# Kernel optimization log

Hardware: AMD Instinct MI355X
Metric: run time of the kernel (lower is better)

The kernel has to match this reference:

```python
import jax, jax.numpy as jnp
import numpy as np

N_NODES = 50000
N_EDGES = 600000
N_GRAPHS = 128
EMB = 128
LAYERS = 5
BN_EPS = 1e-5


def setup_inputs() -> dict:
    key = jax.random.key(0)
    ks = jax.random.split(key, 16)
    inp = {}
    inp['batch'] = jnp.sort(jax.random.randint(ks[0], (N_NODES,), 0, N_GRAPHS)).astype(jnp.int64 if jax.config.jax_enable_x64 else jnp.int32)
    inp['x'] = jax.random.normal(ks[1], (N_NODES, 48), dtype=jnp.float32)
    inp['edge_index'] = jax.random.randint(ks[2], (2, N_EDGES), 0, N_NODES)
    inp['edge_attr'] = jax.random.normal(ks[3], (N_EDGES, 11), dtype=jnp.float32)
    inp['edge_weight'] = jnp.ones((N_EDGES,), dtype=jnp.float32)
    # parameters (xavier-ish scaling)
    inp['W_atom'] = jax.random.normal(ks[4], (48, EMB), dtype=jnp.float32) * (1.0 / np.sqrt(48))
    inp['b_atom'] = jnp.zeros((EMB,), dtype=jnp.float32)
    inp['W_bond'] = jax.random.normal(ks[5], (11, EMB), dtype=jnp.float32) * (1.0 / np.sqrt(11))
    inp['b_bond'] = jnp.zeros((EMB,), dtype=jnp.float32)
    inp['Wl'] = jax.random.normal(ks[6], (LAYERS, EMB, EMB), dtype=jnp.float32) * (1.0 / np.sqrt(EMB))
    inp['bl'] = jnp.zeros((LAYERS, EMB), dtype=jnp.float32)
    inp['Wr'] = jax.random.normal(ks[7], (LAYERS, EMB, EMB), dtype=jnp.float32) * (1.0 / np.sqrt(EMB))
    inp['gamma'] = jnp.ones((LAYERS, EMB), dtype=jnp.float32)
    inp['beta'] = jnp.zeros((LAYERS, EMB), dtype=jnp.float32)
    return inp


def reference(batch, x, edge_index, edge_attr, edge_weight,
              W_atom, b_atom, W_bond, b_bond, Wl, bl, Wr, gamma, beta):
    src = edge_index[0]
    dst = edge_index[1]
    # encoders
    h = x @ W_atom + b_atom                      # [N, EMB]
    ea = edge_attr @ W_bond + b_bond             # [E, EMB]
    # mean-aggregation denominator (in-degree, count-based)
    deg = jax.ops.segment_sum(jnp.ones_like(edge_weight), dst, num_segments=N_NODES)
    denom = jnp.maximum(deg, 1.0)[:, None]       # [N, 1]
    xs = []
    for i in range(LAYERS):
        # SAGEConv: mean over (x_j + edge_attr) * w_e, then lin_l(agg) + lin_r(x)
        msg = (h[src] + ea) * edge_weight[:, None]          # [E, EMB]
        agg = jax.ops.segment_sum(msg, dst, num_segments=N_NODES) / denom
        h = agg @ Wl[i] + bl[i] + h @ Wr[i]
        # BatchNorm1d (training: batch statistics, biased variance)
        mu = jnp.mean(h, axis=0)
        var = jnp.var(h, axis=0)
        h = gamma[i] * (h - mu) * jax.lax.rsqrt(var + BN_EPS) + beta[i]
        if i < LAYERS - 1:
            h = jax.nn.relu(h)
        # dropout with drop_ratio=0.0 is identity
        xs.append(h)
    # layerwise global_add_pool + concat
    xpool = jnp.concatenate(
        [jax.ops.segment_sum(xi, batch, num_segments=N_GRAPHS) for xi in xs], axis=1)
    return (xpool, h)
```

## Files before the change

### kernel.cpp

```cpp
#include <hip/hip_runtime.h>
#include <hip/hip_bf16.h>

#define NNODES 50000
#define NEDGES 600000
#define NGRAPHS 128
#define EMB 128
#define NLAYERS 5
#define BN_EPS 1e-5f
#define SCAN_BLOCKS ((NNODES + 255) / 256)
#define NSB ((NNODES + 255) / 256)
#define EAB ((NNODES + 31) / 32)
#define BPB ((NLAYERS * 32768 + 255) / 256)
#define POOL_CH ((NNODES + 255) / 256)

typedef short s16x8 __attribute__((ext_vector_type(8)));
typedef float f32x16 __attribute__((ext_vector_type(16)));

__device__ __forceinline__ short f2bf(float f) {
    unsigned u = __builtin_bit_cast(unsigned, f);
    unsigned r = (u + 0x7fffu + ((u >> 16) & 1u)) >> 16;
    return (short)r;
}
__device__ __forceinline__ float bf2f(short s) {
    return __builtin_bit_cast(float, ((unsigned)(unsigned short)s) << 16);
}

__global__ __launch_bounds__(256) void init_kernel(float* __restrict__ pool,
                                                   int* __restrict__ deg,
                                                   float* __restrict__ stat) {
    int i = blockIdx.x * 256 + threadIdx.x;
    if (i < NGRAPHS * 640) pool[i] = 0.f;
    if (i < NNODES) deg[i] = 0;
    if (i < NLAYERS * 256) stat[i] = 0.f;
}

__global__ __launch_bounds__(256) void deg_kernel(const int* __restrict__ ei,
                                                  int* __restrict__ deg) {
    int e = blockIdx.x * 256 + threadIdx.x;
    if (e >= NEDGES) return;
    atomicAdd(&deg[ei[NEDGES + e]], 1);
}

__global__ __launch_bounds__(256) void scan1(const int* __restrict__ deg,
                                             int* __restrict__ local_excl,
                                             int* __restrict__ part) {
    __shared__ int sh[256];
    int t = threadIdx.x;
    int i = blockIdx.x * 256 + t;
    int v = (i < NNODES) ? deg[i] : 0;
    sh[t] = v;
    __syncthreads();
    for (int off = 1; off < 256; off <<= 1) {
        int u = (t >= off) ? sh[t - off] : 0;
        __syncthreads();
        sh[t] += u;
        __syncthreads();
    }
    if (i < NNODES) local_excl[i] = sh[t] - v;
    if (t == 255) part[blockIdx.x] = sh[255];
}

__global__ __launch_bounds__(256) void scan23(const int* __restrict__ part,
                                              const int* __restrict__ local_excl,
                                              int* __restrict__ rowptr,
                                              int* __restrict__ cursor) {
    __shared__ int sh[256];
    int t = threadIdx.x;
    int v = (t < SCAN_BLOCKS) ? part[t] : 0;
    sh[t] = v;
    __syncthreads();
    for (int off = 1; off < 256; off <<= 1) {
        int u = (t >= off) ? sh[t - off] : 0;
        __syncthreads();
        sh[t] += u;
        __syncthreads();
    }
    int bo = (blockIdx.x == 0) ? 0 : sh[blockIdx.x - 1];
    int i = blockIdx.x * 256 + t;
    if (i < NNODES) {
        int r = local_excl[i] + bo;
        rowptr[i] = r;
        cursor[i] = r;
    }
    if (blockIdx.x == 0 && t == 0) rowptr[NNODES] = sh[SCAN_BLOCKS - 1];
}

__global__ __launch_bounds__(256) void edge_fill(const int* __restrict__ ei,
                                                 const float* __restrict__ ew,
                                                 const float* __restrict__ eattr,
                                                 int* __restrict__ cursor,
                                                 int* __restrict__ epk) {
    int e = blockIdx.x * 256 + threadIdx.x;
    if (e >= NEDGES) return;
    int src = ei[e];
    int dst = ei[NEDGES + e];
    int pos = atomicAdd(&cursor[dst], 1);
    int pk[8];
    pk[0] = src;
    pk[1] = __float_as_int(ew[e]);
    unsigned short a[12];
#pragma unroll
    for (int j = 0; j < 11; j++) a[j] = (unsigned short)f2bf(eattr[e * 11 + j]);
    a[11] = 0;
#pragma unroll
    for (int j = 0; j < 6; j++)
        pk[2 + j] = (int)a[2 * j] | ((int)a[2 * j + 1] << 16);
    int* dstp = epk + (size_t)pos * 8;
    *(int4*)dstp = *(int4*)pk;
    *(int4*)(dstp + 4) = *(int4*)(pk + 4);
}

__global__ __launch_bounds__(256) void prep2(const int* __restrict__ rowptr,
                                             const int* __restrict__ epk,
                                             int2* __restrict__ epg,
                                             const float* __restrict__ Wb,
                                             const float* __restrict__ bbond,
                                             short* __restrict__ Ehi,
                                             const float* __restrict__ X,
                                             const float* __restrict__ Wa,
                                             const float* __restrict__ ba,
                                             short* __restrict__ Hhi,
                                             const float* __restrict__ Wl,
                                             const float* __restrict__ Wr,
                                             short* __restrict__ Bf) {
    __shared__ float shpool[1792];
    int blk = blockIdx.x;
    int t = threadIdx.x;

    if (blk < NSB) {
        float* Wb_s = shpool;
        float* bb_s = shpool + 1408;
        for (int i = t; i < 1408; i += 256) Wb_s[i] = Wb[i];
        if (t < 128) bb_s[t] = bbond[t];
        __syncthreads();
        int node = blk * 256 + t;
        if (node >= NNODES) return;
        int b = rowptr[node], e = rowptr[node + 1];
        float s[11];
#pragma unroll
        for (int j = 0; j < 11; j++) s[j] = 0.f;
        float ws = 0.f;
        for (int p = b; p < e; p++) {
            const int* pk = epk + (size_t)p * 8;
            int4 lo = *(const int4*)pk;
            int4 hi = *(const int4*)(pk + 4);
            float w = __int_as_float(lo.y);
            ws += w;
            epg[p] = make_int2(lo.x, lo.y);
            int packed[6] = {lo.z, lo.w, hi.x, hi.y, hi.z, hi.w};
#pragma unroll
            for (int j = 0; j < 11; j++) {
                short v = (short)((packed[j >> 1] >> ((j & 1) * 16)) & 0xffff);
                s[j] += bf2f(v) * w;
            }
        }
        short* erow = Ehi + (size_t)node * 128;
#pragma unroll
        for (int c8 = 0; c8 < 16; c8++) {
            s16x8 o;
#pragma unroll
            for (int jj = 0; jj < 8; jj++) {
                int c = c8 * 8 + jj;
                float a = bb_s[c] * ws;
#pragma unroll
                for (int j = 0; j < 11; j++) a += s[j] * Wb_s[j * 128 + c];
                o[jj] = f2bf(a);
            }
            *(s16x8*)(erow + c8 * 8) = o;
        }
    } else if (blk < NSB + EAB) {
        float* as = shpool;
        int row0 = (blk - NSB) * 32;
        for (int i = t; i < 32 * 48; i += 256) {
            int r = i / 48, k = i - r * 48;
            int gr = row0 + r;
            as[k * 36 + r] = (gr < NNODES) ? X[gr * 48 + k] : 0.f;
        }
        __syncthreads();
        int c = t & 127, rh = t >> 7;
        float acc[16];
#pragma unroll
        for (int i = 0; i < 16; i++) acc[i] = 0.f;
        for (int k = 0; k < 48; k++) {
            float w = Wa[k * 128 + c];
            const float* rowv = &as[k * 36 + rh * 16];
            float4 v0 = *(const float4*)(rowv + 0);
            float4 v1 = *(const float4*)(rowv + 4);
            float4 v2 = *(const float4*)(rowv + 8);
            float4 v3 = *(const float4*)(rowv + 12);
            acc[0] += v0.x * w;  acc[1] += v0.y * w;
            acc[2] += v0.z * w;  acc[3] += v0.w * w;
            acc[4] += v1.x * w;  acc[5] += v1.y * w;
            acc[6] += v1.z * w;  acc[7] += v1.w * w;
            acc[8] += v2.x * w;  acc[9] += v2.y * w;
            acc[10] += v2.z * w; acc[11] += v2.w * w;
            acc[12] += v3.x * w; acc[13] += v3.y * w;
            acc[14] += v3.z * w; acc[15] += v3.w * w;
        }
        float bb = ba[c];
        for (int i = 0; i < 16; i++) {
            int gr = row0 + rh * 16 + i;
            if (gr < NNODES) Hhi[(size_t)gr * 128 + c] = f2bf(acc[i] + bb);
        }
    } else {
        int idx = (blk - NSB - EAB) * 256 + t;
        if (idx >= NLAYERS * 32768) return;
        int layer = idx >> 15;
        int r = idx & 32767;
        int k = r >> 7, col = r & 127;
        float w = (k < 128) ? Wl[layer * 16384 + k * 128 + col]
                            : Wr[layer * 16384 + (k - 128) * 128 + col];
        short hi = f2bf(w);
        short lo = f2bf(w - bf2f(hi));
        int ks = k >> 4, half = (k >> 3) & 1, j = k & 7;
        int nt = col >> 5, n32 = col & 31;
        int fo = ((nt * 2 + half) * 32 + n32) * 8 + j;
        short* base = Bf + (size_t)layer * 65536 + ks * 4096;
        base[fo] = hi;
        base[2048 + fo] = lo;
    }
}

__global__ __launch_bounds__(256) void agg_kernel(const short* __restrict__ Hsrc,
                                                  const short* __restrict__ Ehi,
                                                  const int* __restrict__ rowptr,
                                                  const int2* __restrict__ epg,
                                                  const float* __restrict__ stat,
                                                  const float* __restrict__ gamma,
                                                  const float* __restrict__ beta,
                                                  short* __restrict__ Ahi) {
    __shared__ float cscs[128], cshs[128];
    int t = threadIdx.x;
    if (t < 128) {
        float sc = 1.f, sh = 0.f;
        if (stat) {
            const float invM = 1.f / (float)NNODES;
            float mu = stat[t] * invM;
            float var = stat[128 + t] * invM - mu * mu;
            sc = gamma[t] * rsqrtf(var + BN_EPS);
            sh = beta[t] - mu * sc;
        }
        cscs[t] = sc;
        cshs[t] = sh;
    }
    __syncthreads();
    int lane = t & 15, grp = t >> 4;
    int c8 = lane * 8;
    int node = blockIdx.x * 16 + grp;
    if (node >= NNODES) return;
    float rlo = stat ? 0.f : -3.4e38f;
    float sc[8], sh[8];
#pragma unroll
    for (int j = 0; j < 8; j++) { sc[j] = cscs[c8 + j]; sh[j] = cshs[c8 + j]; }
    int b = rowptr[node], e = rowptr[node + 1];
    float s[8];
#pragma unroll
    for (int j = 0; j < 8; j++) s[j] = 0.f;
    int p = b;
    for (; p + 3 < e; p += 4) {
        int2 e0 = epg[p], e1 = epg[p + 1], e2 = epg[p + 2], e3 = epg[p + 3];
        float w0 = __int_as_float(e0.y), w1 = __int_as_float(e1.y);
        float w2 = __int_as_float(e2.y), w3 = __int_as_float(e3.y);
        s16x8 h0 = *(const s16x8*)&Hsrc[(size_t)e0.x * 128 + c8];
        s16x8 h1 = *(const s16x8*)&Hsrc[(size_t)e1.x * 128 + c8];
        s16x8 h2 = *(const s16x8*)&Hsrc[(size_t)e2.x * 128 + c8];
        s16x8 h3 = *(const s16x8*)&Hsrc[(size_t)e3.x * 128 + c8];
#pragma unroll
        for (int j = 0; j < 8; j++) {
            float v0 = fmaxf(bf2f(h0[j]) * sc[j] + sh[j], rlo);
            float v1 = fmaxf(bf2f(h1[j]) * sc[j] + sh[j], rlo);
            float v2 = fmaxf(bf2f(h2[j]) * sc[j] + sh[j], rlo);
            float v3 = fmaxf(bf2f(h3[j]) * sc[j] + sh[j], rlo);
            s[j] += v0 * w0 + v1 * w1 + v2 * w2 + v3 * w3;
        }
    }
    for (; p < e; p++) {
        int2 pk0 = epg[p];
        float w0 = __int_as_float(pk0.y);
        s16x8 h0 = *(const s16x8*)&Hsrc[(size_t)pk0.x * 128 + c8];
#pragma unroll
        for (int j = 0; j < 8; j++)
            s[j] += fmaxf(bf2f(h0[j]) * sc[j] + sh[j], rlo) * w0;
    }
    float inv = 1.f / fmaxf((float)(e - b), 1.f);
    s16x8 ea = *(const s16x8*)&Ehi[(size_t)node * 128 + c8];
    s16x8 o;
#pragma unroll
    for (int j = 0; j < 8; j++) o[j] = f2bf((s[j] + bf2f(ea[j])) * inv);
    *(s16x8*)&Ahi[(size_t)node * 128 + c8] = o;
}

__global__ __launch_bounds__(256) void layer_gemm(const short* __restrict__ Ahi,
                                                  const short* __restrict__ Hsrc,
                                                  const float* __restrict__ statp,
                                                  const float* __restrict__ gamma,
                                                  const float* __restrict__ beta,
                                                  const short* __restrict__ Bf,
                                                  const float* __restrict__ bias,
                                                  short* __restrict__ Cbf,
                                                  float* __restrict__ stat) {
    __shared__ float s_s[128], s_q[128];
    __shared__ float csc[128], csh[128];
    int t = threadIdx.x;
    int wave = t >> 6, lane = t & 63;
    int n32 = lane & 31, half = lane >> 5;
    int rowgrp = wave >> 1, colgrp = wave & 1;
    int row0 = blockIdx.x * 64 + rowgrp * 32;

    if (t < 128) {
        s_s[t] = 0.f;
        s_q[t] = 0.f;
        float sc = 1.f, sh = 0.f;
        if (statp) {
            const float invM = 1.f / (float)NNODES;
            float mu = statp[t] * invM;
            float var = statp[128 + t] * invM - mu * mu;
            sc = gamma[t] * rsqrtf(var + BN_EPS);
            sh = beta[t] - mu * sc;
        }
        csc[t] = sc;
        csh[t] = sh;
    }
    __syncthreads();
    float rlo = statp ? 0.f : -3.4e38f;

    int myrow = row0 + n32;
    bool rowok = myrow < NNODES;
    size_t rbase = (size_t)myrow * 128;
    int acol = half * 8;

    f32x16 acc[2];
#pragma unroll
    for (int i = 0; i < 2; i++) acc[i] = (f32x16)(0.f);

    const short* bb0 = Bf + colgrp * 1024 + half * 256 + n32 * 8;

    s16x8 ahA = {0, 0, 0, 0, 0, 0, 0, 0}, ahB = {0, 0, 0, 0, 0, 0, 0, 0};
    s16x8 bhA[2], blA[2], bhB[2], blB[2];
    if (rowok) {
        ahA = *(const s16x8*)(Ahi + rbase + acol);
        ahB = *(const s16x8*)(Ahi + rbase + 16 + acol);
    }
#pragma unroll
    for (int nt = 0; nt < 2; nt++) {
        bhA[nt] = *(const s16x8*)(bb0 + nt * 512);
        blA[nt] = *(const s16x8*)(bb0 + 2048 + nt * 512);
        bhB[nt] = *(const s16x8*)(bb0 + 4096 + nt * 512);
        blB[nt] = *(const s16x8*)(bb0 + 4096 + 2048 + nt * 512);
    }

#pragma unroll
    for (int ks = 0; ks < 16; ks++) {
        s16x8 ahC = {0, 0, 0, 0, 0, 0, 0, 0};
        s16x8 bhC[2], blC[2];
        if (ks < 14) {
            int kn = ks + 2;
            if (rowok) {
                if (kn < 8) {
                    ahC = *(const s16x8*)(Ahi + rbase + kn * 16 + acol);
                } else {
                    s16x8 hv = *(const s16x8*)(Hsrc + rbase + (kn & 7) * 16 + acol);
                    int kc = (kn & 7) * 16 + acol;
#pragma unroll
                    for (int j = 0; j < 8; j++)
                        ahC[j] = f2bf(fmaxf(bf2f(hv[j]) * csc[kc + j] +
                                            csh[kc + j], rlo));
                }
            }
            const short* bbn = bb0 + kn * 4096;
#pragma unroll
            for (int nt = 0; nt < 2; nt++) {
                bhC[nt] = *(const s16x8*)(bbn + nt * 512);
                blC[nt] = *(const s16x8*)(bbn + 2048 + nt * 512);
            }
        }
#pragma unroll
        for (int nt = 0; nt < 2; nt++) {
            acc[nt] = __builtin_amdgcn_mfma_f32_32x32x16_bf16(ahA, bhA[nt], acc[nt], 0, 0, 0);
            acc[nt] = __builtin_amdgcn_mfma_f32_32x32x16_bf16(ahA, blA[nt], acc[nt], 0, 0, 0);
        }
        ahA = ahB;
        ahB = ahC;
#pragma unroll
        for (int nt = 0; nt < 2; nt++) {
            bhA[nt] = bhB[nt];
            blA[nt] = blB[nt];
            bhB[nt] = bhC[nt];
            blB[nt] = blC[nt];
        }
    }

#pragma unroll
    for (int nt = 0; nt < 2; nt++) {
        int col = colgrp * 64 + nt * 32 + n32;
        float bb = bias[col];
        float ss = 0.f, qq = 0.f;
#pragma unroll
        for (int reg = 0; reg < 16; reg++) {
            int r = row0 + (reg & 3) + 8 * (reg >> 2) + 4 * half;
            if (r < NNODES) {
                float v = acc[nt][reg] + bb;
                Cbf[(size_t)r * 128 + col] = f2bf(v);
                ss += v;
                qq += v * v;
            }
        }
        ss += __shfl_xor(ss, 32);
        qq += __shfl_xor(qq, 32);
        if (half == 0) {
            atomicAdd(&s_s[col], ss);
            atomicAdd(&s_q[col], qq);
        }
    }
    __syncthreads();
    if (t < 128) {
        atomicAdd(&stat[t], s_s[t]);
        atomicAdd(&stat[128 + t], s_q[t]);
    }
}

__global__ __launch_bounds__(256) void pool5(const short* __restrict__ Cbf,
                                             const float* __restrict__ stat,
                                             const float* __restrict__ gamma,
                                             const float* __restrict__ beta,
                                             const int* __restrict__ batch,
                                             float* __restrict__ pool,
                                             float* __restrict__ Hf32) {
    __shared__ float csc[128], csh[128];
    int t = threadIdx.x;
    int u = blockIdx.x;
    int ch = u / NLAYERS, l = u - ch * NLAYERS;
    if (t < 128) {
        const float invM = 1.f / (float)NNODES;
        float mu = stat[l * 256 + t] * invM;
        float var = stat[l * 256 + 128 + t] * invM - mu * mu;
        float sc = gamma[l * 128 + t] * rsqrtf(var + BN_EPS);
        csc[t] = sc;
        csh[t] = beta[l * 128 + t] - mu * sc;
    }
    __syncthreads();
    int lane = t & 31, grp = t >> 5;
    int c4 = lane * 4;
    float4 sc = *(const float4*)&csc[c4];
    float4 sh = *(const float4*)&csh[c4];
    const short* Cl = Cbf + (size_t)l * NNODES * 128;
    int row0 = ch * 256;
    float4 accp = make_float4(0.f, 0.f, 0.f, 0.f);
    int curg = -1;
    float* pbase = pool + l * 128 + c4;
    int relu = (l < NLAYERS - 1);
    for (int rr = grp; rr < 256; rr += 8) {
        int r = row0 + rr;
        if (r >= NNODES) break;
        ushort4 cv = *(const ushort4*)&Cl[(size_t)r * 128 + c4];
        float4 v;
        v.x = bf2f((short)cv.x) * sc.x + sh.x;
        v.y = bf2f((short)cv.y) * sc.y + sh.y;
        v.z = bf2f((short)cv.z) * sc.z + sh.z;
        v.w = bf2f((short)cv.w) * sc.w + sh.w;
        if (relu) {
            v.x = fmaxf(v.x, 0.f);
            v.y = fmaxf(v.y, 0.f);
            v.z = fmaxf(v.z, 0.f);
            v.w = fmaxf(v.w, 0.f);
        } else {
            *(float4*)&Hf32[(size_t)r * 128 + c4] = v;
        }
        int g = batch[r];
        if (g != curg) {
            if (curg >= 0) {
                float* p = pbase + curg * 640;
                atomicAdd(p + 0, accp.x);
                atomicAdd(p + 1, accp.y);
                atomicAdd(p + 2, accp.z);
                atomicAdd(p + 3, accp.w);
            }
            curg = g;
            accp = make_float4(0.f, 0.f, 0.f, 0.f);
        }
        accp.x += v.x;
        accp.y += v.y;
        accp.z += v.z;
        accp.w += v.w;
    }
    if (curg >= 0) {
        float* p = pbase + curg * 640;
        atomicAdd(p + 0, accp.x);
        atomicAdd(p + 1, accp.y);
        atomicAdd(p + 2, accp.z);
        atomicAdd(p + 3, accp.w);
    }
}

extern "C" void kernel_launch(void* const* d_in, const int* in_sizes, int n_in,
                              void* d_out, int out_size, void* d_ws, size_t ws_size,
                              hipStream_t stream) {
    const int* batch = (const int*)d_in[0];
    const float* x = (const float*)d_in[1];
    const int* edge_index = (const int*)d_in[2];
    const float* edge_attr = (const float*)d_in[3];
    const float* edge_weight = (const float*)d_in[4];
    const float* W_atom = (const float*)d_in[5];
    const float* b_atom = (const float*)d_in[6];
    const float* W_bond = (const float*)d_in[7];
    const float* b_bond = (const float*)d_in[8];
    const float* Wl = (const float*)d_in[9];
    const float* bl = (const float*)d_in[10];
    const float* Wr = (const float*)d_in[11];
    const float* gamma = (const float*)d_in[12];
    const float* beta = (const float*)d_in[13];
    float* out = (float*)d_out;

    char* ws = (char*)d_ws;
    size_t off = 0;
    auto alloc = [&](size_t bytes) -> void* {
        void* p = ws + off;
        off += (bytes + 255) & ~(size_t)255;
        return p;
    };
    short* Hhi = (short*)alloc((size_t)NNODES * 128 * 2);
    short* Ahi = (short*)alloc((size_t)NNODES * 128 * 2);
    short* Ehi = (short*)alloc((size_t)NNODES * 128 * 2);
    short* Cbf = (short*)alloc((size_t)NLAYERS * NNODES * 128 * 2);
    int* epk = (int*)alloc((size_t)NEDGES * 32);
    int2* epg = (int2*)alloc((size_t)NEDGES * 8);
    int* rowptr = (int*)alloc((size_t)(NNODES + 1) * 4);
    int* cursor = (int*)alloc((size_t)NNODES * 4);
    int* deg = (int*)alloc((size_t)NNODES * 4);
    float* stat = (float*)alloc(NLAYERS * 256 * 4);
    int* local_excl = (int*)alloc((size_t)NNODES * 4);
    int* part = (int*)alloc(SCAN_BLOCKS * 4);
    short* Bf = (short*)alloc((size_t)NLAYERS * 65536 * 2);

    init_kernel<<<(NGRAPHS * 640 + 255) / 256, 256, 0, stream>>>(out, deg, stat);
    deg_kernel<<<(NEDGES + 255) / 256, 256, 0, stream>>>(edge_index, deg);
    scan1<<<SCAN_BLOCKS, 256, 0, stream>>>(deg, local_excl, part);
    scan23<<<SCAN_BLOCKS, 256, 0, stream>>>(part, local_excl, rowptr, cursor);
    edge_fill<<<(NEDGES + 255) / 256, 256, 0, stream>>>(edge_index, edge_weight,
                                                        edge_attr, cursor, epk);
    prep2<<<NSB + EAB + BPB, 256, 0, stream>>>(rowptr, epk, epg, W_bond, b_bond, Ehi,
                                               x, W_atom, b_atom, Hhi, Wl, Wr, Bf);

    const short* src = Hhi;
    for (int i = 0; i < NLAYERS; i++) {
        const float* st = (i == 0) ? nullptr : stat + (i - 1) * 256;
        const float* gm = (i == 0) ? nullptr : gamma + (i - 1) * 128;
        const float* bt = (i == 0) ? nullptr : beta + (i - 1) * 128;
        short* Ci = Cbf + (size_t)i * NNODES * 128;
        agg_kernel<<<(NNODES + 15) / 16, 256, 0, stream>>>(src, Ehi, rowptr, epg,
                                                           st, gm, bt, Ahi);
        layer_gemm<<<(NNODES + 63) / 64, 256, 0, stream>>>(
            Ahi, src, st, gm, bt, Bf + (size_t)i * 65536, bl + i * 128, Ci,
            stat + i * 256);
        src = Ci;
    }

    pool5<<<POOL_CH * NLAYERS, 256, 0, stream>>>(
        Cbf, stat, gamma, beta, batch, out, out + (size_t)NGRAPHS * 640);
}
```

Before: 588.2 us.

## Widen GEMM tile to full 128 columns, spread BN stat atomics, cache batch ids

The layer GEMM now has each wave compute all 128 output columns for 32 rows, so a block covers 128 rows and the A row fetch and BN-transform work is no longer duplicated across two column groups. The change doubles the accumulator and B-fragment register footprint per wave, which may reduce occupancy. BatchNorm statistic atomics are spread over 8 slots per layer to cut contention, and every reader sums the slots. The pooling kernel also stages batch indices in shared memory before its row loop.

```diff
diff --git a/kernel.cpp b/kernel.cpp
--- a/kernel.cpp
+++ b/kernel.cpp
@@ -7,6 +7,7 @@
 #define EMB 128
 #define NLAYERS 5
 #define BN_EPS 1e-5f
+#define STATW 8
 #define SCAN_BLOCKS ((NNODES + 255) / 256)
 #define NSB ((NNODES + 255) / 256)
 #define EAB ((NNODES + 31) / 32)
@@ -23,6 +24,16 @@
 }
 __device__ __forceinline__ float bf2f(short s) {
     return __builtin_bit_cast(float, ((unsigned)(unsigned short)s) << 16);
+}
+
+__device__ __forceinline__ float2 stat_sum(const float* __restrict__ st, int t) {
+    float s = 0.f, q = 0.f;
+#pragma unroll
+    for (int k = 0; k < STATW; k++) {
+        s += st[k * 256 + t];
+        q += st[k * 256 + 128 + t];
+    }
+    return make_float2(s, q);
 }
 
 __global__ __launch_bounds__(256) void init_kernel(float* __restrict__ pool,
@@ -31,7 +42,7 @@
     int i = blockIdx.x * 256 + threadIdx.x;
     if (i < NGRAPHS * 640) pool[i] = 0.f;
     if (i < NNODES) deg[i] = 0;
-    if (i < NLAYERS * 256) stat[i] = 0.f;
+    if (i < NLAYERS * STATW * 256) stat[i] = 0.f;
 }
 
 __global__ __launch_bounds__(256) void deg_kernel(const int* __restrict__ ei,
@@ -235,8 +246,9 @@
         float sc = 1.f, sh = 0.f;
         if (stat) {
             const float invM = 1.f / (float)NNODES;
-            float mu = stat[t] * invM;
-            float var = stat[128 + t] * invM - mu * mu;
+            float2 sq = stat_sum(stat, t);
+            float mu = sq.x * invM;
+            float var = sq.y * invM - mu * mu;
             sc = gamma[t] * rsqrtf(var + BN_EPS);
             sh = beta[t] - mu * sc;
         }
@@ -304,8 +316,7 @@
     int t = threadIdx.x;
     int wave = t >> 6, lane = t & 63;
     int n32 = lane & 31, half = lane >> 5;
-    int rowgrp = wave >> 1, colgrp = wave & 1;
-    int row0 = blockIdx.x * 64 + rowgrp * 32;
+    int row0 = blockIdx.x * 128 + wave * 32;
 
     if (t < 128) {
         s_s[t] = 0.f;
@@ -313,8 +324,9 @@
         float sc = 1.f, sh = 0.f;
         if (statp) {
             const float invM = 1.f / (float)NNODES;
-            float mu = statp[t] * invM;
-            float var = statp[128 + t] * invM - mu * mu;
+            float2 sq = stat_sum(statp, t);
+            float mu = sq.x * invM;
+            float var = sq.y * invM - mu * mu;
             sc = gamma[t] * rsqrtf(var + BN_EPS);
             sh = beta[t] - mu * sc;
         }
@@ -329,20 +341,20 @@
     size_t rbase = (size_t)myrow * 128;
     int acol = half * 8;
 
-    f32x16 acc[2];
-#pragma unroll
-    for (int i = 0; i < 2; i++) acc[i] = (f32x16)(0.f);
-
-    const short* bb0 = Bf + colgrp * 1024 + half * 256 + n32 * 8;
+    f32x16 acc[4];
+#pragma unroll
+    for (int i = 0; i < 4; i++) acc[i] = (f32x16)(0.f);
+
+    const short* bb0 = Bf + half * 256 + n32 * 8;
 
     s16x8 ahA = {0, 0, 0, 0, 0, 0, 0, 0}, ahB = {0, 0, 0, 0, 0, 0, 0, 0};
-    s16x8 bhA[2], blA[2], bhB[2], blB[2];
+    s16x8 bhA[4], blA[4], bhB[4], blB[4];
     if (rowok) {
         ahA = *(const s16x8*)(Ahi + rbase + acol);
         ahB = *(const s16x8*)(Ahi + rbase + 16 + acol);
     }
 #pragma unroll
-    for (int nt = 0; nt < 2; nt++) {
+    for (int nt = 0; nt < 4; nt++) {
         bhA[nt] = *(const s16x8*)(bb0 + nt * 512);
         blA[nt] = *(const s16x8*)(bb0 + 2048 + nt * 512);
         bhB[nt] = *(const s16x8*)(bb0 + 4096 + nt * 512);
@@ -352,7 +364,7 @@
 #pragma unroll
     for (int ks = 0; ks < 16; ks++) {
         s16x8 ahC = {0, 0, 0, 0, 0, 0, 0, 0};
-        s16x8 bhC[2], blC[2];
+        s16x8 bhC[4], blC[4];
         if (ks < 14) {
             int kn = ks + 2;
             if (rowok) {
@@ -369,20 +381,20 @@
             }
             const short* bbn = bb0 + kn * 4096;
 #pragma unroll
-            for (int nt = 0; nt < 2; nt++) {
+            for (int nt = 0; nt < 4; nt++) {
                 bhC[nt] = *(const s16x8*)(bbn + nt * 512);
                 blC[nt] = *(const s16x8*)(bbn + 2048 + nt * 512);
             }
         }
 #pragma unroll
-        for (int nt = 0; nt < 2; nt++) {
+        for (int nt = 0; nt < 4; nt++) {
             acc[nt] = __builtin_amdgcn_mfma_f32_32x32x16_bf16(ahA, bhA[nt], acc[nt], 0, 0, 0);
             acc[nt] = __builtin_amdgcn_mfma_f32_32x32x16_bf16(ahA, blA[nt], acc[nt], 0, 0, 0);
         }
         ahA = ahB;
         ahB = ahC;
 #pragma unroll
-        for (int nt = 0; nt < 2; nt++) {
+        for (int nt = 0; nt < 4; nt++) {
             bhA[nt] = bhB[nt];
             blA[nt] = blB[nt];
             bhB[nt] = bhC[nt];
@@ -391,8 +403,8 @@
     }
 
 #pragma unroll
-    for (int nt = 0; nt < 2; nt++) {
-        int col = colgrp * 64 + nt * 32 + n32;
+    for (int nt = 0; nt < 4; nt++) {
+        int col = nt * 32 + n32;
         float bb = bias[col];
         float ss = 0.f, qq = 0.f;
 #pragma unroll
@@ -414,8 +426,9 @@
     }
     __syncthreads();
     if (t < 128) {
-        atomicAdd(&stat[t], s_s[t]);
-        atomicAdd(&stat[128 + t], s_q[t]);
+        int slot = blockIdx.x & (STATW - 1);
+        atomicAdd(&stat[slot * 256 + t], s_s[t]);
+        atomicAdd(&stat[slot * 256 + 128 + t], s_q[t]);
     }
 }
 
@@ -427,13 +440,20 @@
                                              float* __restrict__ pool,
                                              float* __restrict__ Hf32) {
     __shared__ float csc[128], csh[128];
+    __shared__ int sbatch[256];
     int t = threadIdx.x;
     int u = blockIdx.x;
     int ch = u / NLAYERS, l = u - ch * NLAYERS;
+    int row0 = ch * 256;
+    {
+        int r = row0 + t;
+        sbatch[t] = (r < NNODES) ? batch[r] : -1;
+    }
     if (t < 128) {
         const float invM = 1.f / (float)NNODES;
-        float mu = stat[l * 256 + t] * invM;
-        float var = stat[l * 256 + 128 + t] * invM - mu * mu;
+        float2 sq = stat_sum(stat + l * STATW * 256, t);
+        float mu = sq.x * invM;
+        float var = sq.y * invM - mu * mu;
         float sc = gamma[l * 128 + t] * rsqrtf(var + BN_EPS);
         csc[t] = sc;
         csh[t] = beta[l * 128 + t] - mu * sc;
@@ -444,7 +464,6 @@
     float4 sc = *(const float4*)&csc[c4];
     float4 sh = *(const float4*)&csh[c4];
     const short* Cl = Cbf + (size_t)l * NNODES * 128;
-    int row0 = ch * 256;
     float4 accp = make_float4(0.f, 0.f, 0.f, 0.f);
     int curg = -1;
     float* pbase = pool + l * 128 + c4;
@@ -466,7 +485,7 @@
         } else {
             *(float4*)&Hf32[(size_t)r * 128 + c4] = v;
         }
-        int g = batch[r];
+        int g = sbatch[rr];
         if (g != curg) {
             if (curg >= 0) {
                 float* p = pbase + curg * 640;
@@ -527,7 +546,7 @@
     int* rowptr = (int*)alloc((size_t)(NNODES + 1) * 4);
     int* cursor = (int*)alloc((size_t)NNODES * 4);
     int* deg = (int*)alloc((size_t)NNODES * 4);
-    float* stat = (float*)alloc(NLAYERS * 256 * 4);
+    float* stat = (float*)alloc(NLAYERS * STATW * 256 * 4);
     int* local_excl = (int*)alloc((size_t)NNODES * 4);
     int* part = (int*)alloc(SCAN_BLOCKS * 4);
     short* Bf = (short*)alloc((size_t)NLAYERS * 65536 * 2);
@@ -543,15 +562,15 @@
 
     const short* src = Hhi;
     for (int i = 0; i < NLAYERS; i++) {
-        const float* st = (i == 0) ? nullptr : stat + (i - 1) * 256;
+        const float* st = (i == 0) ? nullptr : stat + (size_t)(i - 1) * STATW * 256;
         const float* gm = (i == 0) ? nullptr : gamma + (i - 1) * 128;
         const float* bt = (i == 0) ? nullptr : beta + (i - 1) * 128;
         short* Ci = Cbf + (size_t)i * NNODES * 128;
         agg_kernel<<<(NNODES + 15) / 16, 256, 0, stream>>>(src, Ehi, rowptr, epg,
                                                            st, gm, bt, Ahi);
-        layer_gemm<<<(NNODES + 63) / 64, 256, 0, stream>>>(
+        layer_gemm<<<(NNODES + 127) / 128, 256, 0, stream>>>(
             Ahi, src, st, gm, bt, Bf + (size_t)i * 65536, bl + i * 128, Ci,
-            stat + i * 256);
+            stat + (size_t)i * STATW * 256);
         src = Ci;
     }
 
```

Result: faster. 510.2 us (-13.3%).
